# Kernel tuning notes

Hardware: AMD Instinct MI355X
Metric: run time of the kernel (lower is better)

## Reference

```python
import jax, jax.numpy as jnp
import numpy as np

G, B, N, D = 3, 4096, 32, 256
C, H, A, L = 128, 8, 128, 16


def setup_inputs() -> dict:
    key = jax.random.key(0)
    ks = jax.random.split(key, 9)
    return {
        "targets": jax.random.normal(ks[0], (B, D), jnp.float32),
        "contexts": jax.random.normal(ks[1], (G, B, N, D), jnp.float32),
        "kernel": jax.random.normal(ks[2], (D, C), jnp.float32) * 0.05,
        "attn_kernel": jax.random.normal(ks[3], (1, H, 2 * C), jnp.float32) * 0.05,
        "attn_bias": jnp.zeros((H * C,), jnp.float32),
        "sem_kernel": jax.random.normal(ks[4], (H * C, A), jnp.float32) * 0.05,
        "sem_att_kernel": jax.random.normal(ks[5], (A, 1), jnp.float32) * 0.05,
        "dense_w": jax.random.normal(ks[6], (H * C, L), jnp.float32) * 0.05,
        "dense_b": jnp.zeros((L,), jnp.float32),
    }


def reference(targets, contexts, kernel, attn_kernel, attn_bias, sem_kernel,
              sem_att_kernel, dense_w, dense_b):
    # NodeAttention (shared weights across metapath groups; vectorized over G)
    node = jnp.einsum('bd,dc->bc', targets, kernel)            # [B,C]
    neigh = jnp.einsum('gbnd,dc->gbnc', contexts, kernel)      # [G,B,N,C]
    g, b, n, c = neigh.shape
    ak = attn_kernel[0]                                        # [H,2C]
    ak_node, ak_neigh = ak[:, :c], ak[:, c:]                   # split of concat([node, neigh])
    # scores[g,b,n,h] = concat(node_b, neigh_gbn) . ak_h
    scores = (jnp.einsum('bc,hc->bh', node, ak_node)[None, :, None, :]
              + jnp.einsum('gbnc,hc->gbnh', neigh, ak_neigh))  # [G,B,N,H]
    scores = jnp.transpose(scores, (0, 1, 3, 2))               # [G,B,H,N]
    coef = jax.nn.softmax(jax.nn.leaky_relu(scores, 0.2), axis=-1)
    z = jnp.einsum('gbhn,gbnc->gbhc', coef, neigh)             # [G,B,H,C]
    z = z.reshape(g, b, -1) + attn_bias                        # [G,B,H*C] (concat=True)
    # SemanticAttention over metapath groups
    inp = jnp.transpose(z, (1, 0, 2))                          # [B,G,HC]
    s = jnp.squeeze(jnp.matmul(jnp.tanh(jnp.matmul(inp, sem_kernel)), sem_att_kernel), -1)  # [B,G]
    att = jax.nn.softmax(s, axis=-1)
    pooled = jnp.einsum('bg,bgd->bd', att, inp)                # [B,HC]
    logits = pooled @ dense_w + dense_b                        # [B,L]
    return logits
```

## Files before the change

kernel.cpp:

```cpp
#include <hip/hip_runtime.h>
#include <hip/hip_bf16.h>

typedef float v4f __attribute__((ext_vector_type(4)));
typedef short v8s __attribute__((ext_vector_type(8)));

__device__ __forceinline__ unsigned short f2bf(float x){
    unsigned u = __float_as_uint(x);
    u += 0x7FFFu + ((u >> 16) & 1u);
    return (unsigned short)(u >> 16);
}
__device__ __forceinline__ float bf2f(unsigned short h){
    return __uint_as_float(((unsigned)h) << 16);
}
__device__ __forceinline__ v8s pack_bf8(v4f a, v4f b){
    union { v8s s; __hip_bfloat162 h[4]; } u;
    u.h[0] = __float22bfloat162_rn(float2{a[0],a[1]});
    u.h[1] = __float22bfloat162_rn(float2{a[2],a[3]});
    u.h[2] = __float22bfloat162_rn(float2{b[0],b[1]});
    u.h[3] = __float22bfloat162_rn(float2{b[2],b[3]});
    return u.s;
}

__global__ __launch_bounds__(256) void prep_all(const float* __restrict__ targ,
        const float* __restrict__ kern, const float* __restrict__ ak,
        const float* __restrict__ semk, float* __restrict__ ns,
        unsigned short* __restrict__ packB, unsigned short* __restrict__ pack2){
    __shared__ float wsh[256*8];
    int blk = blockIdx.x, t = threadIdx.x;
    if (blk < 16){
        {
            float a[8];
            #pragma unroll
            for (int h=0;h<8;h++) a[h]=0.f;
            const float* kr = kern + t*128;
            for (int c=0;c<128;c++){
                float kv = kr[c];
                #pragma unroll
                for (int h=0;h<8;h++) a[h] = fmaf(kv, ak[h*256+c], a[h]);
            }
            #pragma unroll
            for (int h=0;h<8;h++) wsh[t*8+h]=a[h];
        }
        __syncthreads();
        int b = blk*256 + t;
        float acc[8];
        #pragma unroll
        for (int h=0;h<8;h++) acc[h]=0.f;
        const float* tr = targ + (size_t)b*256;
        for (int d=0;d<256;d++){
            float tv = tr[d];
            #pragma unroll
            for (int h=0;h<8;h++) acc[h] = fmaf(tv, wsh[d*8+h], acc[h]);
        }
        #pragma unroll
        for (int h=0;h<8;h++) ns[b*8+h]=acc[h];
    } else if (blk < 18){
        {
            float a[8];
            #pragma unroll
            for (int h=0;h<8;h++) a[h]=0.f;
            const float* kr = kern + t*128;
            for (int c=0;c<128;c++){
                float kv = kr[c];
                #pragma unroll
                for (int h=0;h<8;h++) a[h] = fmaf(kv, ak[h*256+128+c], a[h]);
            }
            #pragma unroll
            for (int h=0;h<8;h++) wsh[t*8+h]=a[h];
        }
        __syncthreads();
        int gt = (blk-16)*256 + t;
        for (int r=0;r<72;r++){
            int e = gt + r*512;
            int j = e & 7; int l = (e>>3) & 63;
            int fc = e >> 9; int cc = fc % 9; int kk = fc / 9;
            int d = kk*32 + (l>>4)*8 + j;
            int c = cc*16 + (l&15);
            float v;
            if (cc < 8) v = kern[d*128 + c];
            else { int h = c - 128; v = (h < 8) ? wsh[d*8+h] : 0.0f; }
            packB[e] = f2bf(v);
        }
    } else {
        int gt = (blk-18)*256 + t;
        for (int r=0;r<16;r++){
            int e = gt + r*8192;
            int j = e & 7; int l = (e>>3) & 63;
            int cc = (e>>9) & 7; int gkk = e >> 12;
            int k = gkk*32 + (l>>4)*8 + j;
            int a2 = cc*16 + (l&15);
            pack2[e] = f2bf(semk[k*128 + a2]);
        }
    }
}

__global__ __launch_bounds__(256,2) void phase1(const float* __restrict__ ctx,
        const unsigned short* __restrict__ packB, const float* __restrict__ ns,
        const float* __restrict__ bias, unsigned short* __restrict__ zb16){
    __shared__ __align__(16) unsigned short outT[4][32*128];
    __shared__ float cf[4][32*8];

    int t = threadIdx.x, w = t >> 6, lane = t & 63;
    int wt = blockIdx.x*4 + w;
    int g = wt >> 12, b = wt & 4095;
    int q = lane >> 4, h = lane & 15;

    const float* ab = ctx + ((size_t)((g*4096 + b)*32) + h)*256 + q*8;
    const unsigned short* bbase = packB + lane*8;

    v4f acc0[9], acc1[9];
    #pragma unroll
    for (int i=0;i<9;i++){ acc0[i] = (v4f){0.f,0.f,0.f,0.f}; acc1[i] = (v4f){0.f,0.f,0.f,0.f}; }

    #pragma unroll
    for (int kk=0;kk<8;kk++){
        v8s a0 = pack_bf8(*(const v4f*)(ab + kk*32),        *(const v4f*)(ab + kk*32 + 4));
        v8s a1 = pack_bf8(*(const v4f*)(ab + 4096 + kk*32), *(const v4f*)(ab + 4096 + kk*32 + 4));
        #pragma unroll
        for (int cc=0;cc<9;cc++){
            v8s bf = *(const v8s*)(bbase + (kk*9+cc)*512);
            acc0[cc] = __builtin_amdgcn_mfma_f32_16x16x32_bf16(a0, bf, acc0[cc], 0,0,0);
            acc1[cc] = __builtin_amdgcn_mfma_f32_16x16x32_bf16(a1, bf, acc1[cc], 0,0,0);
        }
    }

    {
        float nsv = (h < 8) ? ns[b*8 + h] : 0.f;
        float sc[8];
        #pragma unroll
        for (int r=0;r<4;r++){ sc[r] = acc0[8][r] + nsv; sc[4+r] = acc1[8][r] + nsv; }
        #pragma unroll
        for (int i=0;i<8;i++) sc[i] = sc[i] > 0.f ? sc[i] : 0.2f*sc[i];
        float mx = sc[0];
        #pragma unroll
        for (int i=1;i<8;i++) mx = fmaxf(mx, sc[i]);
        mx = fmaxf(mx, __shfl_xor(mx, 16));
        mx = fmaxf(mx, __shfl_xor(mx, 32));
        float e[8], sum = 0.f;
        #pragma unroll
        for (int i=0;i<8;i++){ e[i] = __expf(sc[i]-mx); sum += e[i]; }
        sum += __shfl_xor(sum, 16);
        sum += __shfl_xor(sum, 32);
        float inv = 1.0f / sum;
        if (h < 8){
            #pragma unroll
            for (int r=0;r<4;r++){
                cf[w][(q*4+r)*8 + h]      = e[r]*inv;
                cf[w][(16+q*4+r)*8 + h]   = e[4+r]*inv;
            }
        }
    }

    #pragma unroll
    for (int cc=0;cc<8;cc++){
        #pragma unroll
        for (int r=0;r<4;r++){
            int row0 = q*4+r, row1 = 16+q*4+r;
            int byte0 = (row0*256 + (cc*16+h)*2) ^ ((row0&7)<<5);
            int byte1 = (row1*256 + (cc*16+h)*2) ^ ((row1&7)<<5);
            *(unsigned short*)((char*)outT[w] + byte0) = f2bf(acc0[cc][r]);
            *(unsigned short*)((char*)outT[w] + byte1) = f2bf(acc1[cc][r]);
        }
    }

    {
        float az0[8], az1[8];
        #pragma unroll
        for (int i=0;i<8;i++){ az0[i]=0.f; az1[i]=0.f; }
        for (int n=0;n<32;n++){
            int byte = (n*256 + lane*4) ^ ((n&7)<<5);
            unsigned v = *(const unsigned*)((const char*)outT[w] + byte);
            float v0 = bf2f((unsigned short)(v & 0xffffu));
            float v1 = bf2f((unsigned short)(v >> 16));
            v4f c0 = *(const v4f*)&cf[w][n*8];
            v4f c1 = *(const v4f*)&cf[w][n*8 + 4];
            az0[0]=fmaf(c0[0],v0,az0[0]); az0[1]=fmaf(c0[1],v0,az0[1]);
            az0[2]=fmaf(c0[2],v0,az0[2]); az0[3]=fmaf(c0[3],v0,az0[3]);
            az0[4]=fmaf(c1[0],v0,az0[4]); az0[5]=fmaf(c1[1],v0,az0[5]);
            az0[6]=fmaf(c1[2],v0,az0[6]); az0[7]=fmaf(c1[3],v0,az0[7]);
            az1[0]=fmaf(c0[0],v1,az1[0]); az1[1]=fmaf(c0[1],v1,az1[1]);
            az1[2]=fmaf(c0[2],v1,az1[2]); az1[3]=fmaf(c0[3],v1,az1[3]);
            az1[4]=fmaf(c1[0],v1,az1[4]); az1[5]=fmaf(c1[1],v1,az1[5]);
            az1[6]=fmaf(c1[2],v1,az1[6]); az1[7]=fmaf(c1[3],v1,az1[7]);
        }
        size_t zb = ((size_t)b*3 + g)*1024;
        int c0i = 2*lane;
        #pragma unroll
        for (int hh=0;hh<8;hh++){
            unsigned short p0 = f2bf(az0[hh] + bias[hh*128 + c0i]);
            unsigned short p1 = f2bf(az1[hh] + bias[hh*128 + c0i + 1]);
            unsigned pk = ((unsigned)p1 << 16) | (unsigned)p0;
            *(unsigned*)(zb16 + zb + hh*128 + c0i) = pk;
        }
    }
}

__global__ __launch_bounds__(256) void semk2(const unsigned short* __restrict__ zb16,
        const unsigned short* __restrict__ pack2, const float* __restrict__ sa,
        float* __restrict__ sws){
    __shared__ float red[16*4];
    int t = threadIdx.x, w = t>>6, lane = t&63;
    int r0 = blockIdx.x * 16;
    v4f acc0 = (v4f){0.f,0.f,0.f,0.f};
    v4f acc1 = (v4f){0.f,0.f,0.f,0.f};
    const unsigned short* abase = zb16 + (size_t)(r0 + (lane&15))*1024 + (lane>>4)*8;
    #pragma unroll 4
    for (int kk=0; kk<32; kk++){
        v8s afr = *(const v8s*)(abase + kk*32);
        v8s b0  = *(const v8s*)(pack2 + (((kk*8 + w  )*64 + lane) << 3));
        v8s b1  = *(const v8s*)(pack2 + (((kk*8 + w+4)*64 + lane) << 3));
        acc0 = __builtin_amdgcn_mfma_f32_16x16x32_bf16(afr, b0, acc0, 0,0,0);
        acc1 = __builtin_amdgcn_mfma_f32_16x16x32_bf16(afr, b1, acc1, 0,0,0);
    }
    float sa0 = sa[w*16 + (lane&15)];
    float sa1 = sa[(w+4)*16 + (lane&15)];
    #pragma unroll
    for (int r=0;r<4;r++){
        float v = fmaf(tanhf(acc0[r]), sa0, tanhf(acc1[r]) * sa1);
        #pragma unroll
        for (int d=1; d<16; d<<=1) v += __shfl_xor(v, d);
        if ((lane&15)==0) red[((lane>>4)*4 + r)*4 + w] = v;
    }
    __syncthreads();
    if (t < 16)
        sws[r0 + t] = red[t*4] + red[t*4+1] + red[t*4+2] + red[t*4+3];
}

__global__ __launch_bounds__(64) void final3(const unsigned short* __restrict__ zb16,
        const float* __restrict__ sws, const float* __restrict__ dw,
        const float* __restrict__ db, float* __restrict__ outp){
    int b = blockIdx.x;
    int lane = threadIdx.x;
    float s0 = sws[b*3], s1 = sws[b*3+1], s2 = sws[b*3+2];
    float m = fmaxf(s0, fmaxf(s1, s2));
    float e0 = __expf(s0-m), e1 = __expf(s1-m), e2 = __expf(s2-m);
    float inv = 1.0f/(e0+e1+e2);
    float a0 = e0*inv, a1 = e1*inv, a2 = e2*inv;

    const unsigned short* z0 = zb16 + (size_t)b*3072 + lane*16;
    v8s za0 = *(const v8s*)(z0);          v8s za1 = *(const v8s*)(z0+8);
    v8s zb0 = *(const v8s*)(z0+1024);     v8s zb1 = *(const v8s*)(z0+1032);
    v8s zc0 = *(const v8s*)(z0+2048);     v8s zc1 = *(const v8s*)(z0+2056);
    float p[16];
    #pragma unroll
    for (int k=0;k<8;k++){
        p[k]   = a0*bf2f((unsigned short)za0[k]) + a1*bf2f((unsigned short)zb0[k]) + a2*bf2f((unsigned short)zc0[k]);
        p[k+8] = a0*bf2f((unsigned short)za1[k]) + a1*bf2f((unsigned short)zb1[k]) + a2*bf2f((unsigned short)zc1[k]);
    }
    float acc[16];
    #pragma unroll
    for (int l=0;l<16;l++) acc[l]=0.f;
    #pragma unroll
    for (int k=0;k<16;k++){
        const float* dr = dw + (lane*16 + k)*16;
        v4f d0 = *(const v4f*)(dr);
        v4f d1 = *(const v4f*)(dr+4);
        v4f d2 = *(const v4f*)(dr+8);
        v4f d3 = *(const v4f*)(dr+12);
        float pk = p[k];
        acc[0]=fmaf(pk,d0[0],acc[0]);  acc[1]=fmaf(pk,d0[1],acc[1]);
        acc[2]=fmaf(pk,d0[2],acc[2]);  acc[3]=fmaf(pk,d0[3],acc[3]);
        acc[4]=fmaf(pk,d1[0],acc[4]);  acc[5]=fmaf(pk,d1[1],acc[5]);
        acc[6]=fmaf(pk,d1[2],acc[6]);  acc[7]=fmaf(pk,d1[3],acc[7]);
        acc[8]=fmaf(pk,d2[0],acc[8]);  acc[9]=fmaf(pk,d2[1],acc[9]);
        acc[10]=fmaf(pk,d2[2],acc[10]); acc[11]=fmaf(pk,d2[3],acc[11]);
        acc[12]=fmaf(pk,d3[0],acc[12]); acc[13]=fmaf(pk,d3[1],acc[13]);
        acc[14]=fmaf(pk,d3[2],acc[14]); acc[15]=fmaf(pk,d3[3],acc[15]);
    }
    #pragma unroll
    for (int l=0;l<16;l++){
        float v = acc[l];
        #pragma unroll
        for (int d=1; d<64; d<<=1) v += __shfl_xor(v, d);
        acc[l] = v;
    }
    float myv = 0.f;
    #pragma unroll
    for (int l=0;l<16;l++) myv = (lane==l) ? acc[l] : myv;
    if (lane < 16) outp[b*16 + lane] = myv + db[lane];
}

extern "C" void kernel_launch(void* const* d_in, const int* in_sizes, int n_in,
                              void* d_out, int out_size, void* d_ws, size_t ws_size,
                              hipStream_t stream) {
    const float* targets  = (const float*)d_in[0];
    const float* contexts = (const float*)d_in[1];
    const float* kern     = (const float*)d_in[2];
    const float* ak       = (const float*)d_in[3];
    const float* bias     = (const float*)d_in[4];
    const float* semk     = (const float*)d_in[5];
    const float* sa       = (const float*)d_in[6];
    const float* dw       = (const float*)d_in[7];
    const float* db       = (const float*)d_in[8];
    float* outp = (float*)d_out;

    char* ws = (char*)d_ws;
    unsigned short* packB = (unsigned short*)(ws);
    float* nsb            = (float*)(ws + 73728);
    unsigned short* pack2 = (unsigned short*)(ws + 204800);
    unsigned short* zb16  = (unsigned short*)(ws + 466944);
    float* sws            = (float*)(ws + 25632768);

    prep_all<<<50, 256, 0, stream>>>(targets, kern, ak, semk, nsb, packB, pack2);
    phase1<<<3072, 256, 0, stream>>>(contexts, packB, nsb, bias, zb16);
    semk2<<<768, 256, 0, stream>>>(zb16, pack2, sa, sws);
    final3<<<4096, 64, 0, stream>>>(zb16, sws, dw, db, outp);
}
```

Before: 197.6 us.

## Compute attention-weighted neighbor sum with MFMA instead of scalar FMA loop

Replaces the scalar 32-step FMA loop that combined softmax coefficients with the neighbor projections by a bf16 MFMA (16x16x32) per 16-channel chunk. Coefficients and the neighbor tile are repacked into transposed bf16 LDS layouts with an 80-byte padded row stride to feed the MFMA fragments. This removes about 512 scalar FMAs plus per-step LDS loads per lane. In exchange, half of the MFMA output is wasted (only 8 of 16 heads used), and the coefficients are now rounded to bf16, which adds precision loss.

New measurement: 203.4 us. 1.03x slower.

```diff
diff --git a/kernel.cpp b/kernel.cpp
--- a/kernel.cpp
+++ b/kernel.cpp
@@ -3,6 +3,7 @@
 
 typedef float v4f __attribute__((ext_vector_type(4)));
 typedef short v8s __attribute__((ext_vector_type(8)));
+typedef short v4s __attribute__((ext_vector_type(4)));
 
 __device__ __forceinline__ unsigned short f2bf(float x){
     unsigned u = __float_as_uint(x);
@@ -18,6 +19,12 @@
     u.h[1] = __float22bfloat162_rn(float2{a[2],a[3]});
     u.h[2] = __float22bfloat162_rn(float2{b[0],b[1]});
     u.h[3] = __float22bfloat162_rn(float2{b[2],b[3]});
+    return u.s;
+}
+__device__ __forceinline__ v4s pack_bf4(v4f a){
+    union { v4s s; __hip_bfloat162 h[2]; } u;
+    u.h[0] = __float22bfloat162_rn(float2{a[0],a[1]});
+    u.h[1] = __float22bfloat162_rn(float2{a[2],a[3]});
     return u.s;
 }
 
@@ -97,15 +104,18 @@
 __global__ __launch_bounds__(256,2) void phase1(const float* __restrict__ ctx,
         const unsigned short* __restrict__ packB, const float* __restrict__ ns,
         const float* __restrict__ bias, unsigned short* __restrict__ zb16){
-    __shared__ __align__(16) unsigned short outT[4][32*128];
-    __shared__ float cf[4][32*8];
+    __shared__ __align__(16) char nT[4][128*80];
+    __shared__ __align__(16) char cT[4][16*80];
 
     int t = threadIdx.x, w = t >> 6, lane = t & 63;
     int wt = blockIdx.x*4 + w;
     int g = wt >> 12, b = wt & 4095;
-    int q = lane >> 4, h = lane & 15;
-
-    const float* ab = ctx + ((size_t)((g*4096 + b)*32) + h)*256 + q*8;
+    int q = lane >> 4, ct = lane & 15;
+
+    char* nTw = nT[w];
+    char* cTw = cT[w];
+
+    const float* ab = ctx + ((size_t)((g*4096 + b)*32) + ct)*256 + q*8;
     const unsigned short* bbase = packB + lane*8;
 
     v4f acc0[9], acc1[9];
@@ -124,8 +134,9 @@
         }
     }
 
+    float einv[8];
     {
-        float nsv = (h < 8) ? ns[b*8 + h] : 0.f;
+        float nsv = (ct < 8) ? ns[b*8 + ct] : 0.f;
         float sc[8];
         #pragma unroll
         for (int r=0;r<4;r++){ sc[r] = acc0[8][r] + nsv; sc[4+r] = acc1[8][r] + nsv; }
@@ -142,55 +153,37 @@
         sum += __shfl_xor(sum, 16);
         sum += __shfl_xor(sum, 32);
         float inv = 1.0f / sum;
-        if (h < 8){
-            #pragma unroll
-            for (int r=0;r<4;r++){
-                cf[w][(q*4+r)*8 + h]      = e[r]*inv;
-                cf[w][(16+q*4+r)*8 + h]   = e[4+r]*inv;
+        #pragma unroll
+        for (int i=0;i<8;i++) einv[i] = e[i]*inv;
+    }
+
+    if (ct < 8){
+        v4f c0 = (v4f){einv[0], einv[1], einv[2], einv[3]};
+        v4f c1 = (v4f){einv[4], einv[5], einv[6], einv[7]};
+        *(v4s*)(cTw + ct*80 + q*8)      = pack_bf4(c0);
+        *(v4s*)(cTw + ct*80 + 32 + q*8) = pack_bf4(c1);
+    }
+
+    #pragma unroll
+    for (int cc=0;cc<8;cc++){
+        char* base = nTw + (cc*16 + ct)*80;
+        *(v4s*)(base + q*8)      = pack_bf4(acc0[cc]);
+        *(v4s*)(base + 32 + q*8) = pack_bf4(acc1[cc]);
+    }
+
+    {
+        v8s bfr = *(const v8s*)(cTw + ct*80 + q*16);
+        size_t zb = ((size_t)b*3 + g)*1024;
+        #pragma unroll
+        for (int m=0;m<8;m++){
+            v8s afr = *(const v8s*)(nTw + (m*16 + ct)*80 + q*16);
+            v4f d = __builtin_amdgcn_mfma_f32_16x16x32_bf16(afr, bfr,
+                        (v4f){0.f,0.f,0.f,0.f}, 0,0,0);
+            if (ct < 8){
+                v4f bv = *(const v4f*)(bias + ct*128 + m*16 + q*4);
+                d[0]+=bv[0]; d[1]+=bv[1]; d[2]+=bv[2]; d[3]+=bv[3];
+                *(v4s*)(zb16 + zb + ct*128 + m*16 + q*4) = pack_bf4(d);
             }
-        }
-    }
-
-    #pragma unroll
-    for (int cc=0;cc<8;cc++){
-        #pragma unroll
-        for (int r=0;r<4;r++){
-            int row0 = q*4+r, row1 = 16+q*4+r;
-            int byte0 = (row0*256 + (cc*16+h)*2) ^ ((row0&7)<<5);
-            int byte1 = (row1*256 + (cc*16+h)*2) ^ ((row1&7)<<5);
-            *(unsigned short*)((char*)outT[w] + byte0) = f2bf(acc0[cc][r]);
-            *(unsigned short*)((char*)outT[w] + byte1) = f2bf(acc1[cc][r]);
-        }
-    }
-
-    {
-        float az0[8], az1[8];
-        #pragma unroll
-        for (int i=0;i<8;i++){ az0[i]=0.f; az1[i]=0.f; }
-        for (int n=0;n<32;n++){
-            int byte = (n*256 + lane*4) ^ ((n&7)<<5);
-            unsigned v = *(const unsigned*)((const char*)outT[w] + byte);
-            float v0 = bf2f((unsigned short)(v & 0xffffu));
-            float v1 = bf2f((unsigned short)(v >> 16));
-            v4f c0 = *(const v4f*)&cf[w][n*8];
-            v4f c1 = *(const v4f*)&cf[w][n*8 + 4];
-            az0[0]=fmaf(c0[0],v0,az0[0]); az0[1]=fmaf(c0[1],v0,az0[1]);
-            az0[2]=fmaf(c0[2],v0,az0[2]); az0[3]=fmaf(c0[3],v0,az0[3]);
-            az0[4]=fmaf(c1[0],v0,az0[4]); az0[5]=fmaf(c1[1],v0,az0[5]);
-            az0[6]=fmaf(c1[2],v0,az0[6]); az0[7]=fmaf(c1[3],v0,az0[7]);
-            az1[0]=fmaf(c0[0],v1,az1[0]); az1[1]=fmaf(c0[1],v1,az1[1]);
-            az1[2]=fmaf(c0[2],v1,az1[2]); az1[3]=fmaf(c0[3],v1,az1[3]);
-            az1[4]=fmaf(c1[0],v1,az1[4]); az1[5]=fmaf(c1[1],v1,az1[5]);
-            az1[6]=fmaf(c1[2],v1,az1[6]); az1[7]=fmaf(c1[3],v1,az1[7]);
-        }
-        size_t zb = ((size_t)b*3 + g)*1024;
-        int c0i = 2*lane;
-        #pragma unroll
-        for (int hh=0;hh<8;hh++){
-            unsigned short p0 = f2bf(az0[hh] + bias[hh*128 + c0i]);
-            unsigned short p1 = f2bf(az1[hh] + bias[hh*128 + c0i + 1]);
-            unsigned pk = ((unsigned)p1 << 16) | (unsigned)p0;
-            *(unsigned*)(zb16 + zb + hh*128 + c0i) = pk;
         }
     }
 }
```

## Make phase1 persistent with double-buffered async global-to-LDS context loads

Applied to the files above, without the earlier changes.

phase1 now launches 512 blocks instead of 3072, and each wave handles 6 (g,b) tiles in a loop. Context rows are fetched with global_load_lds into a per-wave two-slot LDS staging buffer, and the prefetch for chunk k+2 is issued while chunk k is converted and fed to MFMA. The aim is to hide global memory latency on the large contexts stream and cut per-block launch overhead. In exchange it uses extra LDS, relies on hand-written vmcnt/lgkmcnt waits for correctness, and may reduce occupancy or load balance across CUs.

After: 320.0 us. +62.0%, slower.

```diff
diff --git a/kernel.cpp b/kernel.cpp
--- a/kernel.cpp
+++ b/kernel.cpp
@@ -3,6 +3,9 @@
 
 typedef float v4f __attribute__((ext_vector_type(4)));
 typedef short v8s __attribute__((ext_vector_type(8)));
+
+#define AS3(p) ((__attribute__((address_space(3))) void*)(p))
+#define AS1(p) ((__attribute__((address_space(1))) void*)(p))
 
 __device__ __forceinline__ unsigned short f2bf(float x){
     unsigned u = __float_as_uint(x);
@@ -94,103 +97,134 @@
     }
 }
 
+#define P1_ISSUE(SB, TL, KK) {                                                          \
+    const float* r0_ = ctx + ((size_t)(TL)*8192) + (size_t)ct*256 + (KK)*32 + q*8;      \
+    __builtin_amdgcn_global_load_lds(AS1(r0_),      AS3(SB),       16, 0, 0);           \
+    __builtin_amdgcn_global_load_lds(AS1(r0_+4),    AS3((SB)+256), 16, 0, 0);           \
+    __builtin_amdgcn_global_load_lds(AS1(r0_+4096), AS3((SB)+512), 16, 0, 0);           \
+    __builtin_amdgcn_global_load_lds(AS1(r0_+4100), AS3((SB)+768), 16, 0, 0);           \
+}
+
 __global__ __launch_bounds__(256,2) void phase1(const float* __restrict__ ctx,
         const unsigned short* __restrict__ packB, const float* __restrict__ ns,
         const float* __restrict__ bias, unsigned short* __restrict__ zb16){
+    __shared__ __align__(16) float stage[4][2][1024];
     __shared__ __align__(16) unsigned short outT[4][32*128];
     __shared__ float cf[4][32*8];
 
     int t = threadIdx.x, w = t >> 6, lane = t & 63;
-    int wt = blockIdx.x*4 + w;
-    int g = wt >> 12, b = wt & 4095;
-    int q = lane >> 4, h = lane & 15;
-
-    const float* ab = ctx + ((size_t)((g*4096 + b)*32) + h)*256 + q*8;
+    int q = lane >> 4, ct = lane & 15;
+    int wid = blockIdx.x*4 + w;
+    int tbase = wid*6;
+    float* sw0 = &stage[w][0][0];
+    float* sw1 = &stage[w][1][0];
     const unsigned short* bbase = packB + lane*8;
 
-    v4f acc0[9], acc1[9];
-    #pragma unroll
-    for (int i=0;i<9;i++){ acc0[i] = (v4f){0.f,0.f,0.f,0.f}; acc1[i] = (v4f){0.f,0.f,0.f,0.f}; }
-
-    #pragma unroll
-    for (int kk=0;kk<8;kk++){
-        v8s a0 = pack_bf8(*(const v4f*)(ab + kk*32),        *(const v4f*)(ab + kk*32 + 4));
-        v8s a1 = pack_bf8(*(const v4f*)(ab + 4096 + kk*32), *(const v4f*)(ab + 4096 + kk*32 + 4));
-        #pragma unroll
-        for (int cc=0;cc<9;cc++){
-            v8s bf = *(const v8s*)(bbase + (kk*9+cc)*512);
-            acc0[cc] = __builtin_amdgcn_mfma_f32_16x16x32_bf16(a0, bf, acc0[cc], 0,0,0);
-            acc1[cc] = __builtin_amdgcn_mfma_f32_16x16x32_bf16(a1, bf, acc1[cc], 0,0,0);
-        }
-    }
-
-    {
-        float nsv = (h < 8) ? ns[b*8 + h] : 0.f;
-        float sc[8];
-        #pragma unroll
-        for (int r=0;r<4;r++){ sc[r] = acc0[8][r] + nsv; sc[4+r] = acc1[8][r] + nsv; }
-        #pragma unroll
-        for (int i=0;i<8;i++) sc[i] = sc[i] > 0.f ? sc[i] : 0.2f*sc[i];
-        float mx = sc[0];
-        #pragma unroll
-        for (int i=1;i<8;i++) mx = fmaxf(mx, sc[i]);
-        mx = fmaxf(mx, __shfl_xor(mx, 16));
-        mx = fmaxf(mx, __shfl_xor(mx, 32));
-        float e[8], sum = 0.f;
-        #pragma unroll
-        for (int i=0;i<8;i++){ e[i] = __expf(sc[i]-mx); sum += e[i]; }
-        sum += __shfl_xor(sum, 16);
-        sum += __shfl_xor(sum, 32);
-        float inv = 1.0f / sum;
-        if (h < 8){
+    P1_ISSUE(sw0, tbase, 0);
+    P1_ISSUE(sw1, tbase, 1);
+
+    for (int tt=0; tt<6; ++tt){
+        int tl = tbase + tt;
+        int g = tl >> 12, b = tl & 4095;
+
+        v4f acc0[9], acc1[9];
+        #pragma unroll
+        for (int i=0;i<9;i++){ acc0[i] = (v4f){0.f,0.f,0.f,0.f}; acc1[i] = (v4f){0.f,0.f,0.f,0.f}; }
+
+        #pragma unroll
+        for (int kk=0;kk<8;kk++){
+            int ck = tt*8 + kk;
+            float* sb = (ck & 1) ? sw1 : sw0;
+            asm volatile("s_waitcnt vmcnt(4)" ::: "memory");
+            v4f a00 = *(const v4f*)(sb + lane*4);
+            v4f a01 = *(const v4f*)(sb + 256 + lane*4);
+            v4f a10 = *(const v4f*)(sb + 512 + lane*4);
+            v4f a11 = *(const v4f*)(sb + 768 + lane*4);
+            asm volatile("s_waitcnt lgkmcnt(0)" ::: "memory");
+            int ck2 = ck + 2;
+            if (ck2 < 48){
+                int tl2 = tbase + (ck2 >> 3);
+                int kk2 = ck2 & 7;
+                P1_ISSUE(sb, tl2, kk2);
+            }
+            v8s af0 = pack_bf8(a00, a01);
+            v8s af1 = pack_bf8(a10, a11);
+            #pragma unroll
+            for (int cc=0;cc<9;cc++){
+                v8s bf = *(const v8s*)(bbase + (kk*9+cc)*512);
+                acc0[cc] = __builtin_amdgcn_mfma_f32_16x16x32_bf16(af0, bf, acc0[cc], 0,0,0);
+                acc1[cc] = __builtin_amdgcn_mfma_f32_16x16x32_bf16(af1, bf, acc1[cc], 0,0,0);
+            }
+        }
+
+        {
+            float nsv = (ct < 8) ? ns[b*8 + ct] : 0.f;
+            float sc[8];
+            #pragma unroll
+            for (int r=0;r<4;r++){ sc[r] = acc0[8][r] + nsv; sc[4+r] = acc1[8][r] + nsv; }
+            #pragma unroll
+            for (int i=0;i<8;i++) sc[i] = sc[i] > 0.f ? sc[i] : 0.2f*sc[i];
+            float mx = sc[0];
+            #pragma unroll
+            for (int i=1;i<8;i++) mx = fmaxf(mx, sc[i]);
+            mx = fmaxf(mx, __shfl_xor(mx, 16));
+            mx = fmaxf(mx, __shfl_xor(mx, 32));
+            float e[8], sum = 0.f;
+            #pragma unroll
+            for (int i=0;i<8;i++){ e[i] = __expf(sc[i]-mx); sum += e[i]; }
+            sum += __shfl_xor(sum, 16);
+            sum += __shfl_xor(sum, 32);
+            float inv = 1.0f / sum;
+            if (ct < 8){
+                #pragma unroll
+                for (int r=0;r<4;r++){
+                    cf[w][(q*4+r)*8 + ct]    = e[r]*inv;
+                    cf[w][(16+q*4+r)*8 + ct] = e[4+r]*inv;
+                }
+            }
+        }
+
+        #pragma unroll
+        for (int cc=0;cc<8;cc++){
             #pragma unroll
             for (int r=0;r<4;r++){
-                cf[w][(q*4+r)*8 + h]      = e[r]*inv;
-                cf[w][(16+q*4+r)*8 + h]   = e[4+r]*inv;
-            }
-        }
-    }
-
-    #pragma unroll
-    for (int cc=0;cc<8;cc++){
-        #pragma unroll
-        for (int r=0;r<4;r++){
-            int row0 = q*4+r, row1 = 16+q*4+r;
-            int byte0 = (row0*256 + (cc*16+h)*2) ^ ((row0&7)<<5);
-            int byte1 = (row1*256 + (cc*16+h)*2) ^ ((row1&7)<<5);
-            *(unsigned short*)((char*)outT[w] + byte0) = f2bf(acc0[cc][r]);
-            *(unsigned short*)((char*)outT[w] + byte1) = f2bf(acc1[cc][r]);
-        }
-    }
-
-    {
-        float az0[8], az1[8];
-        #pragma unroll
-        for (int i=0;i<8;i++){ az0[i]=0.f; az1[i]=0.f; }
-        for (int n=0;n<32;n++){
-            int byte = (n*256 + lane*4) ^ ((n&7)<<5);
-            unsigned v = *(const unsigned*)((const char*)outT[w] + byte);
-            float v0 = bf2f((unsigned short)(v & 0xffffu));
-            float v1 = bf2f((unsigned short)(v >> 16));
-            v4f c0 = *(const v4f*)&cf[w][n*8];
-            v4f c1 = *(const v4f*)&cf[w][n*8 + 4];
-            az0[0]=fmaf(c0[0],v0,az0[0]); az0[1]=fmaf(c0[1],v0,az0[1]);
-            az0[2]=fmaf(c0[2],v0,az0[2]); az0[3]=fmaf(c0[3],v0,az0[3]);
-            az0[4]=fmaf(c1[0],v0,az0[4]); az0[5]=fmaf(c1[1],v0,az0[5]);
-            az0[6]=fmaf(c1[2],v0,az0[6]); az0[7]=fmaf(c1[3],v0,az0[7]);
-            az1[0]=fmaf(c0[0],v1,az1[0]); az1[1]=fmaf(c0[1],v1,az1[1]);
-            az1[2]=fmaf(c0[2],v1,az1[2]); az1[3]=fmaf(c0[3],v1,az1[3]);
-            az1[4]=fmaf(c1[0],v1,az1[4]); az1[5]=fmaf(c1[1],v1,az1[5]);
-            az1[6]=fmaf(c1[2],v1,az1[6]); az1[7]=fmaf(c1[3],v1,az1[7]);
-        }
-        size_t zb = ((size_t)b*3 + g)*1024;
-        int c0i = 2*lane;
-        #pragma unroll
-        for (int hh=0;hh<8;hh++){
-            unsigned short p0 = f2bf(az0[hh] + bias[hh*128 + c0i]);
-            unsigned short p1 = f2bf(az1[hh] + bias[hh*128 + c0i + 1]);
-            unsigned pk = ((unsigned)p1 << 16) | (unsigned)p0;
-            *(unsigned*)(zb16 + zb + hh*128 + c0i) = pk;
+                int row0 = q*4+r, row1 = 16+q*4+r;
+                int byte0 = (row0*256 + (cc*16+ct)*2) ^ ((row0&7)<<5);
+                int byte1 = (row1*256 + (cc*16+ct)*2) ^ ((row1&7)<<5);
+                *(unsigned short*)((char*)outT[w] + byte0) = f2bf(acc0[cc][r]);
+                *(unsigned short*)((char*)outT[w] + byte1) = f2bf(acc1[cc][r]);
+            }
+        }
+
+        {
+            float az0[8], az1[8];
+            #pragma unroll
+            for (int i=0;i<8;i++){ az0[i]=0.f; az1[i]=0.f; }
+            for (int n=0;n<32;n++){
+                int byte = (n*256 + lane*4) ^ ((n&7)<<5);
+                unsigned v = *(const unsigned*)((const char*)outT[w] + byte);
+                float v0 = bf2f((unsigned short)(v & 0xffffu));
+                float v1 = bf2f((unsigned short)(v >> 16));
+                v4f c0 = *(const v4f*)&cf[w][n*8];
+                v4f c1 = *(const v4f*)&cf[w][n*8 + 4];
+                az0[0]=fmaf(c0[0],v0,az0[0]); az0[1]=fmaf(c0[1],v0,az0[1]);
+                az0[2]=fmaf(c0[2],v0,az0[2]); az0[3]=fmaf(c0[3],v0,az0[3]);
+                az0[4]=fmaf(c1[0],v0,az0[4]); az0[5]=fmaf(c1[1],v0,az0[5]);
+                az0[6]=fmaf(c1[2],v0,az0[6]); az0[7]=fmaf(c1[3],v0,az0[7]);
+                az1[0]=fmaf(c0[0],v1,az1[0]); az1[1]=fmaf(c0[1],v1,az1[1]);
+                az1[2]=fmaf(c0[2],v1,az1[2]); az1[3]=fmaf(c0[3],v1,az1[3]);
+                az1[4]=fmaf(c1[0],v1,az1[4]); az1[5]=fmaf(c1[1],v1,az1[5]);
+                az1[6]=fmaf(c1[2],v1,az1[6]); az1[7]=fmaf(c1[3],v1,az1[7]);
+            }
+            size_t zb = ((size_t)b*3 + g)*1024;
+            int c0i = 2*lane;
+            #pragma unroll
+            for (int hh=0;hh<8;hh++){
+                unsigned short p0 = f2bf(az0[hh] + bias[hh*128 + c0i]);
+                unsigned short p1 = f2bf(az1[hh] + bias[hh*128 + c0i + 1]);
+                unsigned pk = ((unsigned)p1 << 16) | (unsigned)p0;
+                *(unsigned*)(zb16 + zb + hh*128 + c0i) = pk;
+            }
         }
     }
 }
@@ -302,7 +336,7 @@
     float* sws            = (float*)(ws + 25632768);
 
     prep_all<<<50, 256, 0, stream>>>(targets, kern, ak, semk, nsb, packB, pack2);
-    phase1<<<3072, 256, 0, stream>>>(contexts, packB, nsb, bias, zb16);
+    phase1<<<512, 256, 0, stream>>>(contexts, packB, nsb, bias, zb16);
     semk2<<<768, 256, 0, stream>>>(zb16, pack2, sa, sws);
     final3<<<4096, 64, 0, stream>>>(zb16, sws, dw, db, outp);
 }
```

## Stage packed kernel weights in LDS and make phase1 waves loop over targets

Applied to the files above, without the earlier changes.

phase1 now launches 512 blocks of 512 threads. Each block first copies the full packed bf16 weight matrix (72 KB) into shared memory, and each wave then processes three (group, batch) tiles in sequence. B-fragment reads come from LDS instead of global/L2, and that load is amortized over 24 tiles per block. The cost is 144 KB of dynamic shared memory, which allows one block per CU, fewer waves for hiding latency on the streaming context loads, and no large launch attribute is set for the shared-memory size.

Result: slower. 413.0 us (+109.0%).

```diff
diff --git a/kernel.cpp b/kernel.cpp
--- a/kernel.cpp
+++ b/kernel.cpp
@@ -94,103 +94,118 @@
     }
 }
 
-__global__ __launch_bounds__(256,2) void phase1(const float* __restrict__ ctx,
+__global__ __launch_bounds__(512,1) void phase1(const float* __restrict__ ctx,
         const unsigned short* __restrict__ packB, const float* __restrict__ ns,
         const float* __restrict__ bias, unsigned short* __restrict__ zb16){
-    __shared__ __align__(16) unsigned short outT[4][32*128];
-    __shared__ float cf[4][32*8];
+    extern __shared__ __align__(16) char smem[];
+    unsigned short* bl = (unsigned short*)smem;
 
     int t = threadIdx.x, w = t >> 6, lane = t & 63;
-    int wt = blockIdx.x*4 + w;
-    int g = wt >> 12, b = wt & 4095;
-    int q = lane >> 4, h = lane & 15;
-
-    const float* ab = ctx + ((size_t)((g*4096 + b)*32) + h)*256 + q*8;
-    const unsigned short* bbase = packB + lane*8;
-
-    v4f acc0[9], acc1[9];
-    #pragma unroll
-    for (int i=0;i<9;i++){ acc0[i] = (v4f){0.f,0.f,0.f,0.f}; acc1[i] = (v4f){0.f,0.f,0.f,0.f}; }
-
-    #pragma unroll
-    for (int kk=0;kk<8;kk++){
-        v8s a0 = pack_bf8(*(const v4f*)(ab + kk*32),        *(const v4f*)(ab + kk*32 + 4));
-        v8s a1 = pack_bf8(*(const v4f*)(ab + 4096 + kk*32), *(const v4f*)(ab + 4096 + kk*32 + 4));
-        #pragma unroll
-        for (int cc=0;cc<9;cc++){
-            v8s bf = *(const v8s*)(bbase + (kk*9+cc)*512);
-            acc0[cc] = __builtin_amdgcn_mfma_f32_16x16x32_bf16(a0, bf, acc0[cc], 0,0,0);
-            acc1[cc] = __builtin_amdgcn_mfma_f32_16x16x32_bf16(a1, bf, acc1[cc], 0,0,0);
-        }
-    }
+    int q = lane >> 4, ct = lane & 15;
+    unsigned short* outTw = (unsigned short*)(smem + 73728 + w*8192);
+    float* cfw            = (float*)(smem + 73728 + 65536 + w*1024);
 
     {
-        float nsv = (h < 8) ? ns[b*8 + h] : 0.f;
-        float sc[8];
-        #pragma unroll
-        for (int r=0;r<4;r++){ sc[r] = acc0[8][r] + nsv; sc[4+r] = acc1[8][r] + nsv; }
-        #pragma unroll
-        for (int i=0;i<8;i++) sc[i] = sc[i] > 0.f ? sc[i] : 0.2f*sc[i];
-        float mx = sc[0];
-        #pragma unroll
-        for (int i=1;i<8;i++) mx = fmaxf(mx, sc[i]);
-        mx = fmaxf(mx, __shfl_xor(mx, 16));
-        mx = fmaxf(mx, __shfl_xor(mx, 32));
-        float e[8], sum = 0.f;
-        #pragma unroll
-        for (int i=0;i<8;i++){ e[i] = __expf(sc[i]-mx); sum += e[i]; }
-        sum += __shfl_xor(sum, 16);
-        sum += __shfl_xor(sum, 32);
-        float inv = 1.0f / sum;
-        if (h < 8){
+        const v8s* src = (const v8s*)packB;
+        v8s* dst = (v8s*)bl;
+        #pragma unroll
+        for (int r=0;r<9;r++) dst[t + r*512] = src[t + r*512];
+    }
+    __syncthreads();
+
+    const unsigned short* bbase = bl + lane*8;
+    int wid = blockIdx.x*8 + w;
+    int tbase = wid*3;
+
+    for (int tt=0; tt<3; ++tt){
+        int tl = tbase + tt;
+        int g = tl >> 12, b = tl & 4095;
+        const float* ab = ctx + ((size_t)tl*32 + ct)*256 + q*8;
+
+        v4f acc0[9], acc1[9];
+        #pragma unroll
+        for (int i=0;i<9;i++){ acc0[i] = (v4f){0.f,0.f,0.f,0.f}; acc1[i] = (v4f){0.f,0.f,0.f,0.f}; }
+
+        #pragma unroll
+        for (int kk=0;kk<8;kk++){
+            v8s af0 = pack_bf8(*(const v4f*)(ab + kk*32),        *(const v4f*)(ab + kk*32 + 4));
+            v8s af1 = pack_bf8(*(const v4f*)(ab + 4096 + kk*32), *(const v4f*)(ab + 4096 + kk*32 + 4));
+            #pragma unroll
+            for (int cc=0;cc<9;cc++){
+                v8s bf = *(const v8s*)(bbase + (kk*9+cc)*512);
+                acc0[cc] = __builtin_amdgcn_mfma_f32_16x16x32_bf16(af0, bf, acc0[cc], 0,0,0);
+                acc1[cc] = __builtin_amdgcn_mfma_f32_16x16x32_bf16(af1, bf, acc1[cc], 0,0,0);
+            }
+        }
+
+        {
+            float nsv = (ct < 8) ? ns[b*8 + ct] : 0.f;
+            float sc[8];
+            #pragma unroll
+            for (int r=0;r<4;r++){ sc[r] = acc0[8][r] + nsv; sc[4+r] = acc1[8][r] + nsv; }
+            #pragma unroll
+            for (int i=0;i<8;i++) sc[i] = sc[i] > 0.f ? sc[i] : 0.2f*sc[i];
+            float mx = sc[0];
+            #pragma unroll
+            for (int i=1;i<8;i++) mx = fmaxf(mx, sc[i]);
+            mx = fmaxf(mx, __shfl_xor(mx, 16));
+            mx = fmaxf(mx, __shfl_xor(mx, 32));
+            float e[8], sum = 0.f;
+            #pragma unroll
+            for (int i=0;i<8;i++){ e[i] = __expf(sc[i]-mx); sum += e[i]; }
+            sum += __shfl_xor(sum, 16);
+            sum += __shfl_xor(sum, 32);
+            float inv = 1.0f / sum;
+            if (ct < 8){
+                #pragma unroll
+                for (int r=0;r<4;r++){
+                    cfw[(q*4+r)*8 + ct]    = e[r]*inv;
+                    cfw[(16+q*4+r)*8 + ct] = e[4+r]*inv;
+                }
+            }
+        }
+
+        #pragma unroll
+        for (int cc=0;cc<8;cc++){
             #pragma unroll
             for (int r=0;r<4;r++){
-                cf[w][(q*4+r)*8 + h]      = e[r]*inv;
-                cf[w][(16+q*4+r)*8 + h]   = e[4+r]*inv;
-            }
-        }
-    }
-
-    #pragma unroll
-    for (int cc=0;cc<8;cc++){
-        #pragma unroll
-        for (int r=0;r<4;r++){
-            int row0 = q*4+r, row1 = 16+q*4+r;
-            int byte0 = (row0*256 + (cc*16+h)*2) ^ ((row0&7)<<5);
-            int byte1 = (row1*256 + (cc*16+h)*2) ^ ((row1&7)<<5);
-            *(unsigned short*)((char*)outT[w] + byte0) = f2bf(acc0[cc][r]);
-            *(unsigned short*)((char*)outT[w] + byte1) = f2bf(acc1[cc][r]);
-        }
-    }
-
-    {
-        float az0[8], az1[8];
-        #pragma unroll
-        for (int i=0;i<8;i++){ az0[i]=0.f; az1[i]=0.f; }
-        for (int n=0;n<32;n++){
-            int byte = (n*256 + lane*4) ^ ((n&7)<<5);
-            unsigned v = *(const unsigned*)((const char*)outT[w] + byte);
-            float v0 = bf2f((unsigned short)(v & 0xffffu));
-            float v1 = bf2f((unsigned short)(v >> 16));
-            v4f c0 = *(const v4f*)&cf[w][n*8];
-            v4f c1 = *(const v4f*)&cf[w][n*8 + 4];
-            az0[0]=fmaf(c0[0],v0,az0[0]); az0[1]=fmaf(c0[1],v0,az0[1]);
-            az0[2]=fmaf(c0[2],v0,az0[2]); az0[3]=fmaf(c0[3],v0,az0[3]);
-            az0[4]=fmaf(c1[0],v0,az0[4]); az0[5]=fmaf(c1[1],v0,az0[5]);
-            az0[6]=fmaf(c1[2],v0,az0[6]); az0[7]=fmaf(c1[3],v0,az0[7]);
-            az1[0]=fmaf(c0[0],v1,az1[0]); az1[1]=fmaf(c0[1],v1,az1[1]);
-            az1[2]=fmaf(c0[2],v1,az1[2]); az1[3]=fmaf(c0[3],v1,az1[3]);
-            az1[4]=fmaf(c1[0],v1,az1[4]); az1[5]=fmaf(c1[1],v1,az1[5]);
-            az1[6]=fmaf(c1[2],v1,az1[6]); az1[7]=fmaf(c1[3],v1,az1[7]);
-        }
-        size_t zb = ((size_t)b*3 + g)*1024;
-        int c0i = 2*lane;
-        #pragma unroll
-        for (int hh=0;hh<8;hh++){
-            unsigned short p0 = f2bf(az0[hh] + bias[hh*128 + c0i]);
-            unsigned short p1 = f2bf(az1[hh] + bias[hh*128 + c0i + 1]);
-            unsigned pk = ((unsigned)p1 << 16) | (unsigned)p0;
-            *(unsigned*)(zb16 + zb + hh*128 + c0i) = pk;
+                int row0 = q*4+r, row1 = 16+q*4+r;
+                int byte0 = (row0*256 + (cc*16+ct)*2) ^ ((row0&7)<<5);
+                int byte1 = (row1*256 + (cc*16+ct)*2) ^ ((row1&7)<<5);
+                *(unsigned short*)((char*)outTw + byte0) = f2bf(acc0[cc][r]);
+                *(unsigned short*)((char*)outTw + byte1) = f2bf(acc1[cc][r]);
+            }
+        }
+
+        {
+            float az0[8], az1[8];
+            #pragma unroll
+            for (int i=0;i<8;i++){ az0[i]=0.f; az1[i]=0.f; }
+            for (int n=0;n<32;n++){
+                int byte = (n*256 + lane*4) ^ ((n&7)<<5);
+                unsigned v = *(const unsigned*)((const char*)outTw + byte);
+                float v0 = bf2f((unsigned short)(v & 0xffffu));
+                float v1 = bf2f((unsigned short)(v >> 16));
+                v4f c0 = *(const v4f*)&cfw[n*8];
+                v4f c1 = *(const v4f*)&cfw[n*8 + 4];
+                az0[0]=fmaf(c0[0],v0,az0[0]); az0[1]=fmaf(c0[1],v0,az0[1]);
+                az0[2]=fmaf(c0[2],v0,az0[2]); az0[3]=fmaf(c0[3],v0,az0[3]);
+                az0[4]=fmaf(c1[0],v0,az0[4]); az0[5]=fmaf(c1[1],v0,az0[5]);
+                az0[6]=fmaf(c1[2],v0,az0[6]); az0[7]=fmaf(c1[3],v0,az0[7]);
+                az1[0]=fmaf(c0[0],v1,az1[0]); az1[1]=fmaf(c0[1],v1,az1[1]);
+                az1[2]=fmaf(c0[2],v1,az1[2]); az1[3]=fmaf(c0[3],v1,az1[3]);
+                az1[4]=fmaf(c1[0],v1,az1[4]); az1[5]=fmaf(c1[1],v1,az1[5]);
+                az1[6]=fmaf(c1[2],v1,az1[6]); az1[7]=fmaf(c1[3],v1,az1[7]);
+            }
+            size_t zb = ((size_t)b*3 + g)*1024;
+            int c0i = 2*lane;
+            #pragma unroll
+            for (int hh=0;hh<8;hh++){
+                unsigned short p0 = f2bf(az0[hh] + bias[hh*128 + c0i]);
+                unsigned short p1 = f2bf(az1[hh] + bias[hh*128 + c0i + 1]);
+                unsigned pk = ((unsigned)p1 << 16) | (unsigned)p0;
+                *(unsigned*)(zb16 + zb + hh*128 + c0i) = pk;
+            }
         }
     }
 }
@@ -302,7 +317,7 @@
     float* sws            = (float*)(ws + 25632768);
 
     prep_all<<<50, 256, 0, stream>>>(targets, kern, ak, semk, nsb, packB, pack2);
-    phase1<<<3072, 256, 0, stream>>>(contexts, packB, nsb, bias, zb16);
+    phase1<<<512, 512, 147456, stream>>>(contexts, packB, nsb, bias, zb16);
     semk2<<<768, 256, 0, stream>>>(zb16, pack2, sa, sws);
     final3<<<4096, 64, 0, stream>>>(zb16, sws, dw, db, outp);
 }
```
